# Optimization experiments

Measured on AMD Instinct MI355X. Metric: run time of the kernel, lower is better.

## Reference

```python
import jax, jax.numpy as jnp
import numpy as np

N_NODES = 100000
N_EDGES = 1600000
HIDDEN = 128
VOCAB = 1000
N_LAYERS = 3


def setup_inputs() -> dict:
    key = jax.random.key(0)
    ks = jax.random.split(key, 8)
    x = jax.random.randint(ks[0], (N_NODES,), 0, VOCAB)
    edge_index = jax.random.randint(ks[1], (2, N_EDGES), 0, N_NODES)
    s = 1.0 / np.sqrt(HIDDEN)
    emb = jax.random.normal(ks[2], (VOCAB, HIDDEN), dtype=jnp.float32)
    Wl = jax.random.uniform(ks[3], (N_LAYERS, HIDDEN, HIDDEN), minval=-s, maxval=s, dtype=jnp.float32)
    bl = jax.random.uniform(ks[4], (N_LAYERS, HIDDEN), minval=-s, maxval=s, dtype=jnp.float32)
    Wr = jax.random.uniform(ks[5], (N_LAYERS, HIDDEN, HIDDEN), minval=-s, maxval=s, dtype=jnp.float32)
    Wlast = jax.random.uniform(ks[6], (HIDDEN, VOCAB), minval=-s, maxval=s, dtype=jnp.float32)
    blast = jax.random.uniform(ks[7], (VOCAB,), minval=-s, maxval=s, dtype=jnp.float32)
    return {"x": x, "edge_index": edge_index, "emb": emb, "Wl": Wl, "bl": bl,
            "Wr": Wr, "Wlast": Wlast, "blast": blast}


def _sage_conv(h, src, dst, W_l, b_l, W_r, n_nodes):
    # mean-aggregate neighbor (src) features at dst, then transform + root
    msg = h[src]  # [E, H] irregular gather
    agg = jax.ops.segment_sum(msg, dst, num_segments=n_nodes)  # [N, H]
    cnt = jax.ops.segment_sum(jnp.ones((src.shape[0],), h.dtype), dst, num_segments=n_nodes)
    mean = agg / jnp.maximum(cnt, 1.0)[:, None]
    return mean @ W_l + b_l + h @ W_r


def reference(x, edge_index, emb, Wl, bl, Wr, Wlast, blast):
    src, dst = edge_index[0], edge_index[1]
    h = emb[x]  # [N, H] embedding lookup
    for i in range(N_LAYERS):
        h = jax.nn.relu(_sage_conv(h, src, dst, Wl[i], bl[i], Wr[i], N_NODES))
    logits = h @ Wlast + blast  # [N, V]
    return jax.nn.softmax(logits, axis=1)
```

## Files before the change

### kernel.cpp

```cpp
#include <hip/hip_runtime.h>
#include <math.h>

#define N_NODES 100000
#define N_EDGES 1600000
#define HID 128
#define VOCAB 1000
#define ROWSTR 1000
#define NPAD 1024

#define OFF_H0   0
#define OFF_H1   128
#define OFF_COL  256
#define OFF_CNT  768
#define OFF_PTR  769
#define OFF_CUR  770
#define OFF_CSUM 771
#define OFF_COFF 772

#define TNB 8
#define CHUNK 1024
#define NBLK  98

typedef __attribute__((ext_vector_type(8))) short bf16x8;
typedef __attribute__((ext_vector_type(4))) float f32x4;

__device__ __forceinline__ int* meta(float* b, int i, int off) {
    return (int*)(b + (size_t)i * ROWSTR + off);
}
__device__ __forceinline__ int* colp(float* b, int pos) {
    return (int*)(b + (size_t)(pos >> 9) * ROWSTR + OFF_COL + (pos & 511));
}

__device__ __forceinline__ void gload16(const void* g, void* l) {
    __builtin_amdgcn_global_load_lds(
        (const __attribute__((address_space(1))) unsigned int*)g,
        (__attribute__((address_space(3))) unsigned int*)l, 16, 0, 0);
}

__global__ __launch_bounds__(HID) void k_embed(float* __restrict__ base,
                                               const int* __restrict__ x,
                                               const float* __restrict__ emb) {
    int i = blockIdx.x, j = threadIdx.x;
    base[(size_t)i * ROWSTR + OFF_H0 + j] = emb[x[i] * HID + j];
    if (j == 0) *meta(base, i, OFF_CNT) = 0;
}

__global__ __launch_bounds__(256) void k_hist(float* __restrict__ base,
                                              const int* __restrict__ dst) {
    int e = blockIdx.x * 256 + threadIdx.x;
    if (e < N_EDGES) atomicAdd(meta(base, dst[e], OFF_CNT), 1);
}

__global__ __launch_bounds__(256) void k_chunk_sums(float* __restrict__ base) {
    int b = blockIdx.x, t = threadIdx.x;
    int s = 0;
    #pragma unroll
    for (int u = 0; u < 4; ++u) {
        int i = b * CHUNK + t * 4 + u;
        if (i < N_NODES) s += *meta(base, i, OFF_CNT);
    }
    #pragma unroll
    for (int o = 32; o > 0; o >>= 1) s += __shfl_xor(s, o, 64);
    __shared__ int ws[4];
    int wave = t >> 6, lane = t & 63;
    if (lane == 0) ws[wave] = s;
    __syncthreads();
    if (t == 0) *meta(base, b, OFF_CSUM) = ws[0] + ws[1] + ws[2] + ws[3];
}

__global__ void k_scan_top(float* __restrict__ base) {
    if (threadIdx.x == 0) {
        int run = 0;
        for (int b = 0; b < NBLK; ++b) {
            int v = *meta(base, b, OFF_CSUM);
            *meta(base, b, OFF_COFF) = run;
            run += v;
        }
    }
}

__global__ __launch_bounds__(256) void k_scan_apply(float* __restrict__ base) {
    int b = blockIdx.x, t = threadIdx.x;
    int c[4];
    #pragma unroll
    for (int u = 0; u < 4; ++u) {
        int i = b * CHUNK + t * 4 + u;
        c[u] = (i < N_NODES) ? *meta(base, i, OFF_CNT) : 0;
    }
    int tsum = c[0] + c[1] + c[2] + c[3];
    __shared__ int sc[256];
    sc[t] = tsum;
    __syncthreads();
    for (int o = 1; o < 256; o <<= 1) {
        int v = (t >= o) ? sc[t - o] : 0;
        __syncthreads();
        sc[t] += v;
        __syncthreads();
    }
    int start = *meta(base, b, OFF_COFF) + (sc[t] - tsum);
    #pragma unroll
    for (int u = 0; u < 4; ++u) {
        int i = b * CHUNK + t * 4 + u;
        if (i < N_NODES) {
            *meta(base, i, OFF_PTR) = start;
            *meta(base, i, OFF_CUR) = start;
            start += c[u];
        }
    }
}

__global__ __launch_bounds__(256) void k_build(float* __restrict__ base,
                                               const int* __restrict__ src,
                                               const int* __restrict__ dst) {
    int e = blockIdx.x * 256 + threadIdx.x;
    if (e >= N_EDGES) return;
    int pos = atomicAdd(meta(base, dst[e], OFF_CUR), 1);
    *colp(base, pos) = src[e];
}

__global__ __launch_bounds__(HID) void k_layer(float* __restrict__ base,
                                               const float* __restrict__ Wl,
                                               const float* __restrict__ bl,
                                               const float* __restrict__ Wr,
                                               int in_off, int out_off) {
    int j = threadIdx.x;
    int i0 = blockIdx.x * TNB;
    __shared__ __align__(16) float s_m[TNB][HID];
    __shared__ __align__(16) float s_h[TNB][HID];

    for (int r = 0; r < TNB; ++r) {
        int i = i0 + r;
        int beg = *meta(base, i, OFF_PTR);
        int c   = *meta(base, i, OFF_CNT);
        int e = beg, end = beg + c;
        float a0 = 0.f, a1 = 0.f, a2 = 0.f, a3 = 0.f;
        for (; e + 4 <= end; e += 4) {
            int s0 = *colp(base, e + 0);
            int s1 = *colp(base, e + 1);
            int s2 = *colp(base, e + 2);
            int s3 = *colp(base, e + 3);
            a0 += base[(size_t)s0 * ROWSTR + in_off + j];
            a1 += base[(size_t)s1 * ROWSTR + in_off + j];
            a2 += base[(size_t)s2 * ROWSTR + in_off + j];
            a3 += base[(size_t)s3 * ROWSTR + in_off + j];
        }
        for (; e < end; ++e)
            a0 += base[(size_t)(*colp(base, e)) * ROWSTR + in_off + j];
        float a = (a0 + a1) + (a2 + a3);
        s_m[r][j] = a / fmaxf((float)c, 1.0f);
        s_h[r][j] = base[(size_t)i * ROWSTR + in_off + j];
    }
    __syncthreads();

    float acc[TNB];
    #pragma unroll
    for (int r = 0; r < TNB; ++r) acc[r] = 0.f;

    for (int k4 = 0; k4 < HID / 4; ++k4) {
        int k = 4 * k4;
        float wl0 = Wl[(k + 0) * HID + j];
        float wl1 = Wl[(k + 1) * HID + j];
        float wl2 = Wl[(k + 2) * HID + j];
        float wl3 = Wl[(k + 3) * HID + j];
        float wr0 = Wr[(k + 0) * HID + j];
        float wr1 = Wr[(k + 1) * HID + j];
        float wr2 = Wr[(k + 2) * HID + j];
        float wr3 = Wr[(k + 3) * HID + j];
        #pragma unroll
        for (int r = 0; r < TNB; ++r) {
            float4 mv = ((const float4*)s_m[r])[k4];
            float4 hv = ((const float4*)s_h[r])[k4];
            acc[r] += mv.x * wl0 + mv.y * wl1 + mv.z * wl2 + mv.w * wl3
                    + hv.x * wr0 + hv.y * wr1 + hv.z * wr2 + hv.w * wr3;
        }
    }

    float bb = bl[j];
    #pragma unroll
    for (int r = 0; r < TNB; ++r)
        base[(size_t)(i0 + r) * ROWSTR + out_off + j] = fmaxf(acc[r] + bb, 0.f);
}

__global__ __launch_bounds__(256) void k_wsplit(const float* __restrict__ Wlast,
                                                short* __restrict__ Wth,
                                                short* __restrict__ Wtl) {
    int idx = blockIdx.x * 256 + threadIdx.x;
    int k   = idx >> 10;
    int col = idx & (NPAD - 1);
    float f = (col < VOCAB) ? Wlast[(size_t)k * VOCAB + col] : 0.f;
    unsigned b = __float_as_uint(f);
    short hi = (short)(b >> 16);
    float fh = __uint_as_float(b & 0xFFFF0000u);
    short lo = (short)(__float_as_uint(f - fh) >> 16);
    Wth[(size_t)col * HID + k] = hi;
    Wtl[(size_t)col * HID + k] = lo;
}

__global__ __launch_bounds__(512) void k_final_mfma(float* __restrict__ base,
                                                    const short* __restrict__ Wth,
                                                    const short* __restrict__ Wtl,
                                                    const float* __restrict__ blast,
                                                    int h_off) {
    const int t = threadIdx.x;
    const int lane = t & 63, w = t >> 6;
    const int cg = w & 3;
    const int rg = w >> 2;
    const int q = lane >> 4;
    const int i0 = blockIdx.x * 32;

    __shared__ short sW[2][4096 * 8];
    __shared__ float smax[4][32];
    __shared__ float ssum[4][32];

    #pragma unroll
    for (int jj = 0; jj < 8; ++jj) {
        int u = t + jj * 512;
        int col = u & 1023, uq = u >> 10;
        size_t goff = (size_t)col * HID + 0 * 32 + uq * 8;
        gload16(Wth + goff, &sW[0][(size_t)u * 8]);
        gload16(Wtl + goff, &sW[1][(size_t)u * 8]);
    }

    bf16x8 ah[4], al[4];
    {
        const int arow = i0 + rg * 16 + (lane & 15);
        const float* hrow = base + (size_t)arow * ROWSTR + h_off + q * 8;
        #pragma unroll
        for (int kc = 0; kc < 4; ++kc) {
            float4 f0 = ((const float4*)(hrow + kc * 32))[0];
            float4 f1 = ((const float4*)(hrow + kc * 32))[1];
            float f[8] = {f0.x, f0.y, f0.z, f0.w, f1.x, f1.y, f1.z, f1.w};
            #pragma unroll
            for (int u2 = 0; u2 < 8; ++u2) {
                unsigned b = __float_as_uint(f[u2]);
                ah[kc][u2] = (short)(b >> 16);
                float fhv = __uint_as_float(b & 0xFFFF0000u);
                al[kc][u2] = (short)(__float_as_uint(f[u2] - fhv) >> 16);
            }
        }
    }

    f32x4 acc[16];
    #pragma unroll
    for (int tt = 0; tt < 16; ++tt) acc[tt] = (f32x4){0.f, 0.f, 0.f, 0.f};

    #pragma unroll
    for (int kc = 0; kc < 4; ++kc) {
        asm volatile("s_waitcnt vmcnt(0)" ::: "memory");
        __syncthreads();
        #pragma unroll
        for (int tt = 0; tt < 16; ++tt) {
            int col = cg * 256 + tt * 16 + (lane & 15);
            bf16x8 wh = *(const bf16x8*)&sW[0][((size_t)q * 1024 + col) * 8];
            bf16x8 wl = *(const bf16x8*)&sW[1][((size_t)q * 1024 + col) * 8];
            acc[tt] = __builtin_amdgcn_mfma_f32_16x16x32_bf16(ah[kc], wh, acc[tt], 0, 0, 0);
            acc[tt] = __builtin_amdgcn_mfma_f32_16x16x32_bf16(al[kc], wh, acc[tt], 0, 0, 0);
            acc[tt] = __builtin_amdgcn_mfma_f32_16x16x32_bf16(ah[kc], wl, acc[tt], 0, 0, 0);
        }
        if (kc < 3) {
            __syncthreads();
            #pragma unroll
            for (int jj = 0; jj < 8; ++jj) {
                int u = t + jj * 512;
                int col = u & 1023, uq = u >> 10;
                size_t goff = (size_t)col * HID + (kc + 1) * 32 + uq * 8;
                gload16(Wth + goff, &sW[0][(size_t)u * 8]);
                gload16(Wtl + goff, &sW[1][(size_t)u * 8]);
            }
        }
    }

    #pragma unroll
    for (int tt = 0; tt < 16; ++tt) {
        int col = cg * 256 + tt * 16 + (lane & 15);
        float bb = (col < VOCAB) ? blast[col] : 0.f;
        acc[tt][0] += bb; acc[tt][1] += bb; acc[tt][2] += bb; acc[tt][3] += bb;
    }

    float pm[4];
    #pragma unroll
    for (int r = 0; r < 4; ++r) pm[r] = -INFINITY;
    #pragma unroll
    for (int tt = 0; tt < 16; ++tt) {
        int col = cg * 256 + tt * 16 + (lane & 15);
        if (col < VOCAB) {
            #pragma unroll
            for (int r = 0; r < 4; ++r) pm[r] = fmaxf(pm[r], acc[tt][r]);
        }
    }
    #pragma unroll
    for (int s = 1; s < 16; s <<= 1)
        #pragma unroll
        for (int r = 0; r < 4; ++r)
            pm[r] = fmaxf(pm[r], __shfl_xor(pm[r], s, 64));
    if ((lane & 15) == 0) {
        #pragma unroll
        for (int r = 0; r < 4; ++r) smax[cg][rg * 16 + q * 4 + r] = pm[r];
    }
    __syncthreads();
    float M[4];
    #pragma unroll
    for (int r = 0; r < 4; ++r) {
        int row = rg * 16 + q * 4 + r;
        M[r] = fmaxf(fmaxf(smax[0][row], smax[1][row]),
                     fmaxf(smax[2][row], smax[3][row]));
    }

    float ps[4] = {0.f, 0.f, 0.f, 0.f};
    #pragma unroll
    for (int tt = 0; tt < 16; ++tt) {
        int col = cg * 256 + tt * 16 + (lane & 15);
        bool valid = (col < VOCAB);
        #pragma unroll
        for (int r = 0; r < 4; ++r) {
            float e = valid ? __expf(acc[tt][r] - M[r]) : 0.f;
            acc[tt][r] = e;
            ps[r] += e;
        }
    }
    #pragma unroll
    for (int s = 1; s < 16; s <<= 1)
        #pragma unroll
        for (int r = 0; r < 4; ++r)
            ps[r] += __shfl_xor(ps[r], s, 64);
    if ((lane & 15) == 0) {
        #pragma unroll
        for (int r = 0; r < 4; ++r) ssum[cg][rg * 16 + q * 4 + r] = ps[r];
    }
    __syncthreads();
    float inv[4];
    #pragma unroll
    for (int r = 0; r < 4; ++r) {
        int row = rg * 16 + q * 4 + r;
        float S = (ssum[0][row] + ssum[1][row]) + (ssum[2][row] + ssum[3][row]);
        inv[r] = 1.0f / S;
    }

    #pragma unroll
    for (int tt = 0; tt < 16; ++tt) {
        int col = cg * 256 + tt * 16 + (lane & 15);
        if (col < VOCAB) {
            #pragma unroll
            for (int r = 0; r < 4; ++r) {
                int row = i0 + rg * 16 + q * 4 + r;
                base[(size_t)row * ROWSTR + col] = acc[tt][r] * inv[r];
            }
        }
    }
}

extern "C" void kernel_launch(void* const* d_in, const int* in_sizes, int n_in,
                              void* d_out, int out_size, void* d_ws, size_t ws_size,
                              hipStream_t stream) {
    (void)in_sizes; (void)n_in; (void)out_size; (void)ws_size;
    const int*   x     = (const int*)d_in[0];
    const int*   ei    = (const int*)d_in[1];
    const float* emb   = (const float*)d_in[2];
    const float* Wl    = (const float*)d_in[3];
    const float* bl    = (const float*)d_in[4];
    const float* Wr    = (const float*)d_in[5];
    const float* Wlast = (const float*)d_in[6];
    const float* blast = (const float*)d_in[7];
    float* base = (float*)d_out;
    const int* src = ei;
    const int* dst = ei + N_EDGES;

    short* Wth = (short*)d_ws;
    short* Wtl = Wth + (size_t)NPAD * HID;

    const int EG = (N_EDGES + 255) / 256;

    k_wsplit<<<dim3(NPAD * HID / 256), dim3(256), 0, stream>>>(Wlast, Wth, Wtl);
    k_embed<<<dim3(N_NODES), dim3(HID), 0, stream>>>(base, x, emb);
    k_hist<<<dim3(EG), dim3(256), 0, stream>>>(base, dst);
    k_chunk_sums<<<dim3(NBLK), dim3(256), 0, stream>>>(base);
    k_scan_top<<<dim3(1), dim3(64), 0, stream>>>(base);
    k_scan_apply<<<dim3(NBLK), dim3(256), 0, stream>>>(base);
    k_build<<<dim3(EG), dim3(256), 0, stream>>>(base, src, dst);

    int in_off = OFF_H0, out_off = OFF_H1;
    for (int l = 0; l < 3; ++l) {
        k_layer<<<dim3(N_NODES / TNB), dim3(HID), 0, stream>>>(
            base, Wl + (size_t)l * HID * HID, bl + (size_t)l * HID,
            Wr + (size_t)l * HID * HID, in_off, out_off);
        int tmp = in_off; in_off = out_off; out_off = tmp;
    }
    k_final_mfma<<<dim3(N_NODES / 32), dim3(512), 0, stream>>>(
        base, Wth, Wtl, blast, in_off);
}
```

Before: 1.868 ms.

## Warp-per-row gather with prefetch, pre-swizzled weights, double-buffered MFMA and staged stores

Result: faster. 1.542 ms (-17.4%).

```diff
diff --git a/kernel.cpp b/kernel.cpp
--- a/kernel.cpp
+++ b/kernel.cpp
@@ -118,44 +118,66 @@
     *colp(base, pos) = src[e];
 }
 
-__global__ __launch_bounds__(HID) void k_layer(float* __restrict__ base,
+__global__ __launch_bounds__(256) void k_layer(float* __restrict__ base,
                                                const float* __restrict__ Wl,
                                                const float* __restrict__ bl,
                                                const float* __restrict__ Wr,
                                                int in_off, int out_off) {
-    int j = threadIdx.x;
-    int i0 = blockIdx.x * TNB;
+    const int t = threadIdx.x;
+    const int wv = t >> 6, lane = t & 63;
+    const int i0 = blockIdx.x * TNB;
     __shared__ __align__(16) float s_m[TNB][HID];
     __shared__ __align__(16) float s_h[TNB][HID];
 
-    for (int r = 0; r < TNB; ++r) {
-        int i = i0 + r;
+    #pragma unroll
+    for (int rr = 0; rr < TNB / 4; ++rr) {
+        const int r = rr * 4 + wv;
+        const int i = i0 + r;
         int beg = *meta(base, i, OFF_PTR);
         int c   = *meta(base, i, OFF_CNT);
         int e = beg, end = beg + c;
-        float a0 = 0.f, a1 = 0.f, a2 = 0.f, a3 = 0.f;
-        for (; e + 4 <= end; e += 4) {
-            int s0 = *colp(base, e + 0);
-            int s1 = *colp(base, e + 1);
-            int s2 = *colp(base, e + 2);
-            int s3 = *colp(base, e + 3);
-            a0 += base[(size_t)s0 * ROWSTR + in_off + j];
-            a1 += base[(size_t)s1 * ROWSTR + in_off + j];
-            a2 += base[(size_t)s2 * ROWSTR + in_off + j];
-            a3 += base[(size_t)s3 * ROWSTR + in_off + j];
-        }
-        for (; e < end; ++e)
-            a0 += base[(size_t)(*colp(base, e)) * ROWSTR + in_off + j];
-        float a = (a0 + a1) + (a2 + a3);
-        s_m[r][j] = a / fmaxf((float)c, 1.0f);
-        s_h[r][j] = base[(size_t)i * ROWSTR + in_off + j];
-    }
-    __syncthreads();
-
-    float acc[TNB];
-    #pragma unroll
-    for (int r = 0; r < TNB; ++r) acc[r] = 0.f;
-
+        float ax0=0.f, ay0=0.f, ax1=0.f, ay1=0.f;
+        float ax2=0.f, ay2=0.f, ax3=0.f, ay3=0.f;
+        int sA0=0, sA1=0, sA2=0, sA3=0;
+        bool have = (e + 4 <= end);
+        if (have) {
+            sA0 = *colp(base, e + 0); sA1 = *colp(base, e + 1);
+            sA2 = *colp(base, e + 2); sA3 = *colp(base, e + 3);
+        }
+        while (have) {
+            bool haveN = (e + 8 <= end);
+            int n0=0, n1=0, n2=0, n3=0;
+            if (haveN) {
+                n0 = *colp(base, e + 4); n1 = *colp(base, e + 5);
+                n2 = *colp(base, e + 6); n3 = *colp(base, e + 7);
+            }
+            float2 v0 = *(const float2*)&base[(size_t)sA0 * ROWSTR + in_off + 2 * lane];
+            float2 v1 = *(const float2*)&base[(size_t)sA1 * ROWSTR + in_off + 2 * lane];
+            float2 v2 = *(const float2*)&base[(size_t)sA2 * ROWSTR + in_off + 2 * lane];
+            float2 v3 = *(const float2*)&base[(size_t)sA3 * ROWSTR + in_off + 2 * lane];
+            ax0 += v0.x; ay0 += v0.y; ax1 += v1.x; ay1 += v1.y;
+            ax2 += v2.x; ay2 += v2.y; ax3 += v3.x; ay3 += v3.y;
+            e += 4;
+            sA0 = n0; sA1 = n1; sA2 = n2; sA3 = n3;
+            have = haveN;
+        }
+        for (; e < end; ++e) {
+            int s = *colp(base, e);
+            float2 v = *(const float2*)&base[(size_t)s * ROWSTR + in_off + 2 * lane];
+            ax0 += v.x; ay0 += v.y;
+        }
+        float invc = 1.0f / fmaxf((float)c, 1.0f);
+        s_m[r][2 * lane + 0] = (ax0 + ax1 + ax2 + ax3) * invc;
+        s_m[r][2 * lane + 1] = (ay0 + ay1 + ay2 + ay3) * invc;
+        float2 hv = *(const float2*)&base[(size_t)i * ROWSTR + in_off + 2 * lane];
+        s_h[r][2 * lane + 0] = hv.x;
+        s_h[r][2 * lane + 1] = hv.y;
+    }
+    __syncthreads();
+
+    const int j = t & 127;
+    const int r0 = (t >> 7) * 4;
+    float acc[4] = {0.f, 0.f, 0.f, 0.f};
     for (int k4 = 0; k4 < HID / 4; ++k4) {
         int k = 4 * k4;
         float wl0 = Wl[(k + 0) * HID + j];
@@ -167,38 +189,44 @@
         float wr2 = Wr[(k + 2) * HID + j];
         float wr3 = Wr[(k + 3) * HID + j];
         #pragma unroll
-        for (int r = 0; r < TNB; ++r) {
-            float4 mv = ((const float4*)s_m[r])[k4];
-            float4 hv = ((const float4*)s_h[r])[k4];
+        for (int r = 0; r < 4; ++r) {
+            float4 mv = ((const float4*)s_m[r0 + r])[k4];
+            float4 hv = ((const float4*)s_h[r0 + r])[k4];
             acc[r] += mv.x * wl0 + mv.y * wl1 + mv.z * wl2 + mv.w * wl3
                     + hv.x * wr0 + hv.y * wr1 + hv.z * wr2 + hv.w * wr3;
         }
     }
-
     float bb = bl[j];
     #pragma unroll
-    for (int r = 0; r < TNB; ++r)
-        base[(size_t)(i0 + r) * ROWSTR + out_off + j] = fmaxf(acc[r] + bb, 0.f);
+    for (int r = 0; r < 4; ++r)
+        base[(size_t)(i0 + r0 + r) * ROWSTR + out_off + j] = fmaxf(acc[r] + bb, 0.f);
 }
 
 __global__ __launch_bounds__(256) void k_wsplit(const float* __restrict__ Wlast,
-                                                short* __restrict__ Wth,
-                                                short* __restrict__ Wtl) {
-    int idx = blockIdx.x * 256 + threadIdx.x;
-    int k   = idx >> 10;
-    int col = idx & (NPAD - 1);
-    float f = (col < VOCAB) ? Wlast[(size_t)k * VOCAB + col] : 0.f;
-    unsigned b = __float_as_uint(f);
-    short hi = (short)(b >> 16);
-    float fh = __uint_as_float(b & 0xFFFF0000u);
-    short lo = (short)(__float_as_uint(f - fh) >> 16);
-    Wth[(size_t)col * HID + k] = hi;
-    Wtl[(size_t)col * HID + k] = lo;
+                                                short* __restrict__ Wsw) {
+    int u = blockIdx.x * 256 + threadIdx.x;
+    int col = u & 1023;
+    int q   = (u >> 10) & 3;
+    int s   = u >> 12;
+    int kc = s >> 1, half = s & 1;
+    bf16x8 v;
+    #pragma unroll
+    for (int i = 0; i < 8; ++i) {
+        int k = kc * 32 + q * 8 + i;
+        float f = (col < VOCAB) ? Wlast[(size_t)k * VOCAB + col] : 0.f;
+        unsigned b = __float_as_uint(f);
+        if (half == 0) {
+            v[i] = (short)(b >> 16);
+        } else {
+            float fh = __uint_as_float(b & 0xFFFF0000u);
+            v[i] = (short)(__float_as_uint(f - fh) >> 16);
+        }
+    }
+    *(bf16x8*)&Wsw[(size_t)u * 8] = v;
 }
 
 __global__ __launch_bounds__(512) void k_final_mfma(float* __restrict__ base,
-                                                    const short* __restrict__ Wth,
-                                                    const short* __restrict__ Wtl,
+                                                    const short* __restrict__ Wsw,
                                                     const float* __restrict__ blast,
                                                     int h_off) {
     const int t = threadIdx.x;
@@ -206,24 +234,18 @@
     const int cg = w & 3;
     const int rg = w >> 2;
     const int q = lane >> 4;
+    const int lr = lane & 15;
     const int i0 = blockIdx.x * 32;
 
-    __shared__ short sW[2][4096 * 8];
+    __shared__ __align__(16) char smem[133120];
+    short* sW = (short*)smem;
+    float* sF = (float*)smem;
     __shared__ float smax[4][32];
     __shared__ float ssum[4][32];
 
-    #pragma unroll
-    for (int jj = 0; jj < 8; ++jj) {
-        int u = t + jj * 512;
-        int col = u & 1023, uq = u >> 10;
-        size_t goff = (size_t)col * HID + 0 * 32 + uq * 8;
-        gload16(Wth + goff, &sW[0][(size_t)u * 8]);
-        gload16(Wtl + goff, &sW[1][(size_t)u * 8]);
-    }
-
     bf16x8 ah[4], al[4];
     {
-        const int arow = i0 + rg * 16 + (lane & 15);
+        const int arow = i0 + rg * 16 + lr;
         const float* hrow = base + (size_t)arow * ROWSTR + h_off + q * 8;
         #pragma unroll
         for (int kc = 0; kc < 4; ++kc) {
@@ -234,45 +256,56 @@
             for (int u2 = 0; u2 < 8; ++u2) {
                 unsigned b = __float_as_uint(f[u2]);
                 ah[kc][u2] = (short)(b >> 16);
-                float fhv = __uint_as_float(b & 0xFFFF0000u);
-                al[kc][u2] = (short)(__float_as_uint(f[u2] - fhv) >> 16);
+                float fh = __uint_as_float(b & 0xFFFF0000u);
+                al[kc][u2] = (short)(__float_as_uint(f[u2] - fh) >> 16);
             }
         }
     }
 
+    #define STAGEU(s, b) { \
+        const short* gsrc = Wsw + (size_t)(s) * 32768; \
+        short* ldst = sW + (size_t)(b) * 32768; \
+        _Pragma("unroll") \
+        for (int jj = 0; jj < 8; ++jj) { \
+            int uu = t + jj * 512; \
+            gload16(gsrc + (size_t)uu * 8, ldst + (size_t)uu * 8); \
+        } }
+
+    STAGEU(0, 0);
+    STAGEU(1, 1);
+
     f32x4 acc[16];
     #pragma unroll
     for (int tt = 0; tt < 16; ++tt) acc[tt] = (f32x4){0.f, 0.f, 0.f, 0.f};
 
     #pragma unroll
-    for (int kc = 0; kc < 4; ++kc) {
-        asm volatile("s_waitcnt vmcnt(0)" ::: "memory");
-        __syncthreads();
+    for (int u = 0; u < 8; ++u) {
+        if (u < 7) asm volatile("s_waitcnt vmcnt(8)" ::: "memory");
+        else       asm volatile("s_waitcnt vmcnt(0)" ::: "memory");
+        __builtin_amdgcn_s_barrier();
+        const short* B = sW + (size_t)(u & 1) * 32768;
+        const int kc = u >> 1;
+        __builtin_amdgcn_s_setprio(1);
         #pragma unroll
         for (int tt = 0; tt < 16; ++tt) {
-            int col = cg * 256 + tt * 16 + (lane & 15);
-            bf16x8 wh = *(const bf16x8*)&sW[0][((size_t)q * 1024 + col) * 8];
-            bf16x8 wl = *(const bf16x8*)&sW[1][((size_t)q * 1024 + col) * 8];
-            acc[tt] = __builtin_amdgcn_mfma_f32_16x16x32_bf16(ah[kc], wh, acc[tt], 0, 0, 0);
-            acc[tt] = __builtin_amdgcn_mfma_f32_16x16x32_bf16(al[kc], wh, acc[tt], 0, 0, 0);
-            acc[tt] = __builtin_amdgcn_mfma_f32_16x16x32_bf16(ah[kc], wl, acc[tt], 0, 0, 0);
-        }
-        if (kc < 3) {
-            __syncthreads();
-            #pragma unroll
-            for (int jj = 0; jj < 8; ++jj) {
-                int u = t + jj * 512;
-                int col = u & 1023, uq = u >> 10;
-                size_t goff = (size_t)col * HID + (kc + 1) * 32 + uq * 8;
-                gload16(Wth + goff, &sW[0][(size_t)u * 8]);
-                gload16(Wtl + goff, &sW[1][(size_t)u * 8]);
+            int col = cg * 256 + tt * 16 + lr;
+            bf16x8 wv = *(const bf16x8*)&B[((size_t)q * 1024 + col) * 8];
+            if ((u & 1) == 0) {
+                acc[tt] = __builtin_amdgcn_mfma_f32_16x16x32_bf16(ah[kc], wv, acc[tt], 0, 0, 0);
+                acc[tt] = __builtin_amdgcn_mfma_f32_16x16x32_bf16(al[kc], wv, acc[tt], 0, 0, 0);
+            } else {
+                acc[tt] = __builtin_amdgcn_mfma_f32_16x16x32_bf16(ah[kc], wv, acc[tt], 0, 0, 0);
             }
         }
-    }
+        __builtin_amdgcn_s_setprio(0);
+        __builtin_amdgcn_s_barrier();
+        if (u + 2 < 8) { STAGEU(u + 2, u & 1); }
+    }
+    #undef STAGEU
 
     #pragma unroll
     for (int tt = 0; tt < 16; ++tt) {
-        int col = cg * 256 + tt * 16 + (lane & 15);
+        int col = cg * 256 + tt * 16 + lr;
         float bb = (col < VOCAB) ? blast[col] : 0.f;
         acc[tt][0] += bb; acc[tt][1] += bb; acc[tt][2] += bb; acc[tt][3] += bb;
     }
@@ -282,7 +315,7 @@
     for (int r = 0; r < 4; ++r) pm[r] = -INFINITY;
     #pragma unroll
     for (int tt = 0; tt < 16; ++tt) {
-        int col = cg * 256 + tt * 16 + (lane & 15);
+        int col = cg * 256 + tt * 16 + lr;
         if (col < VOCAB) {
             #pragma unroll
             for (int r = 0; r < 4; ++r) pm[r] = fmaxf(pm[r], acc[tt][r]);
@@ -293,7 +326,7 @@
         #pragma unroll
         for (int r = 0; r < 4; ++r)
             pm[r] = fmaxf(pm[r], __shfl_xor(pm[r], s, 64));
-    if ((lane & 15) == 0) {
+    if (lr == 0) {
         #pragma unroll
         for (int r = 0; r < 4; ++r) smax[cg][rg * 16 + q * 4 + r] = pm[r];
     }
@@ -309,7 +342,7 @@
     float ps[4] = {0.f, 0.f, 0.f, 0.f};
     #pragma unroll
     for (int tt = 0; tt < 16; ++tt) {
-        int col = cg * 256 + tt * 16 + (lane & 15);
+        int col = cg * 256 + tt * 16 + lr;
         bool valid = (col < VOCAB);
         #pragma unroll
         for (int r = 0; r < 4; ++r) {
@@ -323,7 +356,7 @@
         #pragma unroll
         for (int r = 0; r < 4; ++r)
             ps[r] += __shfl_xor(ps[r], s, 64);
-    if ((lane & 15) == 0) {
+    if (lr == 0) {
         #pragma unroll
         for (int r = 0; r < 4; ++r) ssum[cg][rg * 16 + q * 4 + r] = ps[r];
     }
@@ -338,14 +371,20 @@
 
     #pragma unroll
     for (int tt = 0; tt < 16; ++tt) {
-        int col = cg * 256 + tt * 16 + (lane & 15);
-        if (col < VOCAB) {
-            #pragma unroll
-            for (int r = 0; r < 4; ++r) {
-                int row = i0 + rg * 16 + q * 4 + r;
-                base[(size_t)row * ROWSTR + col] = acc[tt][r] * inv[r];
-            }
-        }
+        int col = cg * 256 + tt * 16 + lr;
+        #pragma unroll
+        for (int r = 0; r < 4; ++r) {
+            int row = rg * 16 + q * 4 + r;
+            sF[row * 1040 + col] = acc[tt][r] * inv[r];
+        }
+    }
+    __syncthreads();
+
+    for (int idx = t; idx < 32 * 250; idx += 512) {
+        int row = idx / 250;
+        int c4  = idx - row * 250;
+        float4 v = *(const float4*)&sF[row * 1040 + c4 * 4];
+        *(float4*)&base[(size_t)(i0 + row) * ROWSTR + c4 * 4] = v;
     }
 }
 
@@ -365,12 +404,11 @@
     const int* src = ei;
     const int* dst = ei + N_EDGES;
 
-    short* Wth = (short*)d_ws;
-    short* Wtl = Wth + (size_t)NPAD * HID;
+    short* Wsw = (short*)d_ws;
 
     const int EG = (N_EDGES + 255) / 256;
 
-    k_wsplit<<<dim3(NPAD * HID / 256), dim3(256), 0, stream>>>(Wlast, Wth, Wtl);
+    k_wsplit<<<dim3(128), dim3(256), 0, stream>>>(Wlast, Wsw);
     k_embed<<<dim3(N_NODES), dim3(HID), 0, stream>>>(base, x, emb);
     k_hist<<<dim3(EG), dim3(256), 0, stream>>>(base, dst);
     k_chunk_sums<<<dim3(NBLK), dim3(256), 0, stream>>>(base);
@@ -380,11 +418,11 @@
 
     int in_off = OFF_H0, out_off = OFF_H1;
     for (int l = 0; l < 3; ++l) {
-        k_layer<<<dim3(N_NODES / TNB), dim3(HID), 0, stream>>>(
+        k_layer<<<dim3(N_NODES / TNB), dim3(256), 0, stream>>>(
             base, Wl + (size_t)l * HID * HID, bl + (size_t)l * HID,
             Wr + (size_t)l * HID * HID, in_off, out_off);
         int tmp = in_off; in_off = out_off; out_off = tmp;
     }
     k_final_mfma<<<dim3(N_NODES / 32), dim3(512), 0, stream>>>(
-        base, Wth, Wtl, blast, in_off);
-}
+        base, Wsw, blast, in_off);
+}
```
